# Optimization experiments

Hardware: AMD Instinct MI355X
Metric: run time of the kernel (lower is better)

The kernel has to match this reference:

```python
import jax, jax.numpy as jnp
import numpy as np

B, C, H, W = 8, 128, 64, 64
CQK = C // 8


def setup_inputs() -> dict:
    key = jax.random.key(0)
    ks = jax.random.split(key, 7)
    scale = 1.0 / np.sqrt(C)
    return {
        "x": jax.random.normal(ks[0], (B, C, H, W), dtype=jnp.float32),
        "wq": jax.random.normal(ks[1], (CQK, C), dtype=jnp.float32) * scale,
        "bq": jax.random.normal(ks[2], (CQK,), dtype=jnp.float32) * 0.01,
        "wk": jax.random.normal(ks[3], (CQK, C), dtype=jnp.float32) * scale,
        "bk": jax.random.normal(ks[4], (CQK,), dtype=jnp.float32) * 0.01,
        "wv": jax.random.normal(ks[5], (C, C), dtype=jnp.float32) * scale,
        "bv": jax.random.normal(ks[6], (C,), dtype=jnp.float32) * 0.01,
    }


def reference(x, wq, bq, wk, bk, wv, bv):
    b, c, h, w = x.shape
    n = h * w
    xf = x.reshape(b, c, n)                                  # [B,C,N]
    # 1x1 convs == channel matmuls
    q = jnp.einsum('oc,bcn->bon', wq, xf) + bq[:, None]      # [B,C/8,N]
    k = jnp.einsum('oc,bcn->bon', wk, xf) + bk[:, None]      # [B,C/8,N]
    v = jnp.einsum('oc,bcn->bon', wv, xf) + bv[:, None]      # [B,C,N]
    # energy[b,i,j] = <q[:,i], k[:,j]>  (note: NO 1/sqrt(d) scale, per source)
    energy = jnp.einsum('bci,bcj->bij', q, k)                # [B,N,N]
    att = jax.nn.softmax(energy, axis=-1)                    # softmax over j
    # out[b,c,i] = sum_j v[b,c,j] * att[b,i,j]
    out = jnp.einsum('bcj,bij->bci', v, att).reshape(b, c, h, w)
    return out + x
```

## Files before the change

kernel.cpp:

```cpp
#include <hip/hip_runtime.h>
#include <math.h>

#define NB  8
#define NC  128
#define NN  4096
#define NCQ 16
#define BI  64
#define BJ  64
#define NT  (NN / BJ)
#define WROWS 160

typedef __attribute__((ext_vector_type(8))) short short8v;
typedef __attribute__((ext_vector_type(4))) short short4v;
typedef __attribute__((ext_vector_type(4))) float f32x4;

__device__ __forceinline__ short f2bf(float f) {
    unsigned u = __builtin_bit_cast(unsigned, f);
    u += 0x7fffu + ((u >> 16) & 1u);
    return (short)(u >> 16);
}
__device__ __forceinline__ float bf2f(short h) {
    return __builtin_bit_cast(float, ((unsigned)(unsigned short)h) << 16);
}

__global__ __launch_bounds__(256) void wconv(
    const float* __restrict__ wq, const float* __restrict__ bq,
    const float* __restrict__ wk, const float* __restrict__ bk,
    const float* __restrict__ wv, const float* __restrict__ bv,
    short* __restrict__ whg, short* __restrict__ wlg, float* __restrict__ biasg)
{
    const int idx = blockIdx.x * 256 + threadIdx.x;
    if (idx < WROWS * NC) {
        const int row = idx >> 7, k = idx & 127;
        const float v = (row < 16) ? wq[row * NC + k]
                       : (row < 32) ? wk[(row - 16) * NC + k]
                                    : wv[(row - 32) * NC + k];
        const short h = f2bf(v);
        whg[idx] = h;
        wlg[idx] = f2bf(v - bf2f(h));
    }
    if (idx < WROWS)
        biasg[idx] = (idx < 16) ? bq[idx] : (idx < 32) ? bk[idx - 16] : bv[idx - 32];
}

__global__ __launch_bounds__(256) void qkv_gemm(
    const float* __restrict__ x,
    const short* __restrict__ whg, const short* __restrict__ wlg,
    const float* __restrict__ biasg,
    short* __restrict__ Qo, short* __restrict__ Ko, short* __restrict__ Vo)
{
    __shared__ __align__(16) short xsT[2][64][136];

    const int b  = blockIdx.y;
    const int n0 = blockIdx.x * 64;
    const int t  = threadIdx.x;
    const int w  = t >> 6;
    const int l  = t & 63;
    const int lr = l & 15;
    const int g  = l >> 4;

    const float* xb = x + (size_t)b * NC * NN;

#pragma unroll
    for (int it = 0; it < 8; ++it) {
        const int idx4 = t + 256 * it;
        const int cr = idx4 >> 4;
        const int j4 = (idx4 & 15) * 4;
        const float4 v = *reinterpret_cast<const float4*>(xb + (size_t)cr * NN + n0 + j4);
        const float vf[4] = {v.x, v.y, v.z, v.w};
#pragma unroll
        for (int p = 0; p < 4; ++p) {
            const short h = f2bf(vf[p]);
            xsT[0][j4 + p][cr] = h;
            xsT[1][j4 + p][cr] = f2bf(vf[p] - bf2f(h));
        }
    }
    __syncthreads();

    const int lc = 16 * w + lr;
    f32x4 acc[10];
#pragma unroll
    for (int rt = 0; rt < 10; ++rt) acc[rt] = {0.f, 0.f, 0.f, 0.f};

#pragma unroll
    for (int ks = 0; ks < 4; ++ks) {
        const short8v xh = *reinterpret_cast<const short8v*>(&xsT[0][lc][32 * ks + 8 * g]);
        const short8v xl = *reinterpret_cast<const short8v*>(&xsT[1][lc][32 * ks + 8 * g]);
#pragma unroll
        for (int rt = 0; rt < 10; ++rt) {
            const int wo = (16 * rt + lr) * NC + 32 * ks + 8 * g;
            const short8v ah = *reinterpret_cast<const short8v*>(whg + wo);
            const short8v al = *reinterpret_cast<const short8v*>(wlg + wo);
            acc[rt] = __builtin_amdgcn_mfma_f32_16x16x32_bf16(ah, xh, acc[rt], 0, 0, 0);
            acc[rt] = __builtin_amdgcn_mfma_f32_16x16x32_bf16(ah, xl, acc[rt], 0, 0, 0);
            acc[rt] = __builtin_amdgcn_mfma_f32_16x16x32_bf16(al, xh, acc[rt], 0, 0, 0);
        }
    }

    const int col = n0 + lc;
#pragma unroll
    for (int rt = 0; rt < 10; ++rt) {
#pragma unroll
        for (int r = 0; r < 4; ++r) {
            const int ch = 16 * rt + 4 * g + r;
            const short o = f2bf(acc[rt][r] + biasg[ch]);
            if (rt == 0)
                Qo[((size_t)b * NCQ + ch) * NN + col] = o;
            else if (rt == 1)
                Ko[((size_t)b * NCQ + (ch - 16)) * NN + col] = o;
            else
                Vo[((size_t)b * NC + (ch - 32)) * NN + col] = o;
        }
    }
}

__global__ __launch_bounds__(256) void attn_mfma(
    const short* __restrict__ Q, const short* __restrict__ K,
    const short* __restrict__ V, const float* __restrict__ x,
    float* __restrict__ out)
{
    __shared__ __align__(16) short ksT[2][BJ * 24];
    __shared__ __align__(16) short vsT[3][NC * BJ];
    __shared__ __align__(16) short psT[4][2][16 * BJ];

    const int b  = blockIdx.y;
    const int i0 = blockIdx.x * BI;
    const int t  = threadIdx.x;
    const int w  = t >> 6;
    const int l  = t & 63;
    const int lr = l & 15;
    const int g  = l >> 4;
    const int swz = (lr & 7) << 3;

    const short* Qb = Q + (size_t)b * NCQ * NN;
    const short* Kb = K + (size_t)b * NCQ * NN;
    const short* Vb = V + (size_t)b * NC * NN;

    const int ig = i0 + 16 * w + lr;

    const short8v kzero = {0, 0, 0, 0, 0, 0, 0, 0};
    const f32x4   fzero = {0.f, 0.f, 0.f, 0.f};

    const int kc  = t >> 4;
    const int kj4 = (t & 15) * 4;
    const int vc0 = t >> 3;
    const int vj8 = (t & 7) * 8;

    short4v kreg;
    short8v vreg0, vreg1, vreg2, vreg3;

#define LOAD_TILE(J0)                                                            \
    {                                                                            \
        kreg  = *reinterpret_cast<const short4v*>(Kb + (size_t)kc * NN + (J0) + kj4); \
        vreg0 = *reinterpret_cast<const short8v*>(Vb + (size_t)(vc0      ) * NN + (J0) + vj8); \
        vreg1 = *reinterpret_cast<const short8v*>(Vb + (size_t)(vc0 + 32 ) * NN + (J0) + vj8); \
        vreg2 = *reinterpret_cast<const short8v*>(Vb + (size_t)(vc0 + 64 ) * NN + (J0) + vj8); \
        vreg3 = *reinterpret_cast<const short8v*>(Vb + (size_t)(vc0 + 96 ) * NN + (J0) + vj8); \
    }
#define WRITE_TILE(KB_, VB_)                                                     \
    {                                                                            \
        _Pragma("unroll")                                                        \
        for (int p = 0; p < 4; ++p) ksT[KB_][(kj4 + p) * 24 + kc] = kreg[p];     \
        const int sw0 = vj8 ^ ((vc0 & 7) << 3);                                  \
        *reinterpret_cast<short8v*>(&vsT[VB_][(vc0      ) * BJ + sw0]) = vreg0;  \
        *reinterpret_cast<short8v*>(&vsT[VB_][(vc0 + 32 ) * BJ + sw0]) = vreg1;  \
        *reinterpret_cast<short8v*>(&vsT[VB_][(vc0 + 64 ) * BJ + sw0]) = vreg2;  \
        *reinterpret_cast<short8v*>(&vsT[VB_][(vc0 + 96 ) * BJ + sw0]) = vreg3;  \
    }
#define PV_STEP(PB_, VB_)                                                        \
    {                                                                            \
        __builtin_amdgcn_s_setprio(1);                                           \
        _Pragma("unroll")                                                        \
        for (int ks = 0; ks < 2; ++ks) {                                         \
            const int jb = (32 * ks + 8 * g) ^ swz;                              \
            const short8v pf = *reinterpret_cast<const short8v*>(                \
                    &psT[w][PB_][lr * BJ + jb]);                                 \
            _Pragma("unroll")                                                    \
            for (int cb = 0; cb < 8; ++cb) {                                     \
                const short8v vf = *reinterpret_cast<const short8v*>(            \
                        &vsT[VB_][(16 * cb + lr) * BJ + jb]);                    \
                acc[cb] = __builtin_amdgcn_mfma_f32_16x16x32_bf16(vf, pf, acc[cb], 0, 0, 0); \
            }                                                                    \
        }                                                                        \
        __builtin_amdgcn_s_setprio(0);                                           \
    }

    short8v qf = kzero;
    if (g < 2) {
        const short* qp = Qb + (size_t)(8 * g) * NN + ig;
#pragma unroll
        for (int e = 0; e < 8; ++e) qf[e] = qp[(size_t)e * NN];
    }

    float l_run = 0.f;
    f32x4 acc[8];
#pragma unroll
    for (int cb = 0; cb < 8; ++cb) acc[cb] = fzero;

    LOAD_TILE(0)
    WRITE_TILE(0, 0)
    __syncthreads();

    int vwr = 1;
    int vpv = 0;

    for (int jt = 0; jt < NT; ++jt) {
        const int kcur = jt & 1;
        if (jt < NT - 1) LOAD_TILE((jt + 1) * BJ)

        f32x4 e0, e1, e2, e3;
#define QK_TILE(ET, TT)                                                          \
        {                                                                        \
            short8v kf = kzero;                                                  \
            if (g < 2)                                                           \
                kf = *reinterpret_cast<const short8v*>(                          \
                        &ksT[kcur][(16 * (TT) + lr) * 24 + 8 * g]);              \
            ET = __builtin_amdgcn_mfma_f32_16x16x32_bf16(kf, qf, fzero, 0, 0, 0);\
        }
        QK_TILE(e0, 0) QK_TILE(e1, 1) QK_TILE(e2, 2) QK_TILE(e3, 3)
#undef QK_TILE

        float sum = 0.f;
#pragma unroll
        for (int r = 0; r < 4; ++r) { e0[r] = __expf(e0[r]); sum += e0[r]; }
#pragma unroll
        for (int r = 0; r < 4; ++r) { e1[r] = __expf(e1[r]); sum += e1[r]; }
#pragma unroll
        for (int r = 0; r < 4; ++r) { e2[r] = __expf(e2[r]); sum += e2[r]; }
#pragma unroll
        for (int r = 0; r < 4; ++r) { e3[r] = __expf(e3[r]); sum += e3[r]; }
        sum += __shfl_xor(sum, 16);
        sum += __shfl_xor(sum, 32);
        l_run += sum;

#define P_STORE(ET, TT)                                                           \
        {                                                                         \
            const int jb = 16 * (TT) + 4 * g;                                     \
            unsigned p01 = (unsigned short)f2bf(ET[0]) |                          \
                           ((unsigned)(unsigned short)f2bf(ET[1]) << 16);         \
            unsigned p23 = (unsigned short)f2bf(ET[2]) |                          \
                           ((unsigned)(unsigned short)f2bf(ET[3]) << 16);         \
            *reinterpret_cast<unsigned*>(&psT[w][kcur][lr * BJ + ( jb      ^ swz)]) = p01; \
            *reinterpret_cast<unsigned*>(&psT[w][kcur][lr * BJ + ((jb + 2) ^ swz)]) = p23; \
        }
        P_STORE(e0, 0) P_STORE(e1, 1) P_STORE(e2, 2) P_STORE(e3, 3)
#undef P_STORE

        if (jt > 0) {
            PV_STEP(kcur ^ 1, vpv)
            vpv = (vpv == 2) ? 0 : vpv + 1;
        }

        if (jt < NT - 1) {
            WRITE_TILE(kcur ^ 1, vwr)
            vwr = (vwr == 2) ? 0 : vwr + 1;
        }
        __syncthreads();
    }

    PV_STEP((NT - 1) & 1, vpv)

#undef LOAD_TILE
#undef WRITE_TILE
#undef PV_STEP

    const float inv = 1.f / l_run;
#pragma unroll
    for (int cb = 0; cb < 8; ++cb) {
#pragma unroll
        for (int r = 0; r < 4; ++r) {
            const int c = 16 * cb + 4 * g + r;
            const size_t o = ((size_t)b * NC + c) * NN + ig;
            out[o] = acc[cb][r] * inv + x[o];
        }
    }
}

extern "C" void kernel_launch(void* const* d_in, const int* in_sizes, int n_in,
                              void* d_out, int out_size, void* d_ws, size_t ws_size,
                              hipStream_t stream) {
    const float* x  = (const float*)d_in[0];
    const float* wq = (const float*)d_in[1];
    const float* bq = (const float*)d_in[2];
    const float* wk = (const float*)d_in[3];
    const float* bk = (const float*)d_in[4];
    const float* wv = (const float*)d_in[5];
    const float* bv = (const float*)d_in[6];
    float* out = (float*)d_out;

    short* ws = (short*)d_ws;
    short* Qo  = ws;
    short* Ko  = ws + (size_t)NB * NCQ * NN;
    short* Vo  = ws + 2 * (size_t)NB * NCQ * NN;
    short* whg = ws + 10 * (size_t)NB * NCQ * NN;
    short* wlg = whg + WROWS * NC;
    float* biasg = (float*)(wlg + WROWS * NC);

    wconv<<<dim3(80), 256, 0, stream>>>(wq, bq, wk, bk, wv, bv, whg, wlg, biasg);
    qkv_gemm<<<dim3(NN / 64, NB), 256, 0, stream>>>(x, whg, wlg, biasg, Qo, Ko, Vo);
    attn_mfma<<<dim3(NN / BI, NB), 256, 0, stream>>>(Qo, Ko, Vo, x, out);
}
```

Baseline: 193.3 us.

## Split attention work across waves by key tile and channel, read K/V directly from global

K is now written transposed ([N,16]) by the QKV GEMM, so each wave can load its K fragment straight from global memory. In the attention kernel each wave now computes energies for its own 16-column slice of the key tile against all 64 query rows. It shares P through LDS and does the PV product for a 32-channel slice, with V fragments loaded straight from global instead of staged in LDS. This removes the K/V LDS staging and the large vsT buffers and should raise occupancy. In exchange it adds uncoalesced V/K global loads per wave and a cross-wave row-sum reduction through LDS at the end.

```diff
diff --git a/kernel.cpp b/kernel.cpp
--- a/kernel.cpp
+++ b/kernel.cpp
@@ -47,7 +47,7 @@
     const float* __restrict__ x,
     const short* __restrict__ whg, const short* __restrict__ wlg,
     const float* __restrict__ biasg,
-    short* __restrict__ Qo, short* __restrict__ Ko, short* __restrict__ Vo)
+    short* __restrict__ Qo, short* __restrict__ KoT, short* __restrict__ Vo)
 {
     __shared__ __align__(16) short xsT[2][64][136];
 
@@ -107,7 +107,7 @@
             if (rt == 0)
                 Qo[((size_t)b * NCQ + ch) * NN + col] = o;
             else if (rt == 1)
-                Ko[((size_t)b * NCQ + (ch - 16)) * NN + col] = o;
+                KoT[((size_t)b * NN + col) * NCQ + (ch - 16)] = o;
             else
                 Vo[((size_t)b * NC + (ch - 32)) * NN + col] = o;
         }
@@ -115,13 +115,12 @@
 }
 
 __global__ __launch_bounds__(256) void attn_mfma(
-    const short* __restrict__ Q, const short* __restrict__ K,
+    const short* __restrict__ Q, const short* __restrict__ KT,
     const short* __restrict__ V, const float* __restrict__ x,
     float* __restrict__ out)
 {
-    __shared__ __align__(16) short ksT[2][BJ * 24];
-    __shared__ __align__(16) short vsT[3][NC * BJ];
-    __shared__ __align__(16) short psT[4][2][16 * BJ];
+    __shared__ __align__(16) short psT[2][64][72];
+    __shared__ float lsumX[4][4][16];
 
     const int b  = blockIdx.y;
     const int i0 = blockIdx.x * BI;
@@ -130,148 +129,153 @@
     const int l  = t & 63;
     const int lr = l & 15;
     const int g  = l >> 4;
-    const int swz = (lr & 7) << 3;
-
-    const short* Qb = Q + (size_t)b * NCQ * NN;
-    const short* Kb = K + (size_t)b * NCQ * NN;
-    const short* Vb = V + (size_t)b * NC * NN;
-
-    const int ig = i0 + 16 * w + lr;
+
+    const short* Qb  = Q  + (size_t)b * NCQ * NN;
+    const short* KTb = KT + (size_t)b * NN * NCQ;
+    const short* Vb  = V  + (size_t)b * NC * NN;
 
     const short8v kzero = {0, 0, 0, 0, 0, 0, 0, 0};
     const f32x4   fzero = {0.f, 0.f, 0.f, 0.f};
 
-    const int kc  = t >> 4;
-    const int kj4 = (t & 15) * 4;
-    const int vc0 = t >> 3;
-    const int vj8 = (t & 7) * 8;
-
-    short4v kreg;
-    short8v vreg0, vreg1, vreg2, vreg3;
-
-#define LOAD_TILE(J0)                                                            \
-    {                                                                            \
-        kreg  = *reinterpret_cast<const short4v*>(Kb + (size_t)kc * NN + (J0) + kj4); \
-        vreg0 = *reinterpret_cast<const short8v*>(Vb + (size_t)(vc0      ) * NN + (J0) + vj8); \
-        vreg1 = *reinterpret_cast<const short8v*>(Vb + (size_t)(vc0 + 32 ) * NN + (J0) + vj8); \
-        vreg2 = *reinterpret_cast<const short8v*>(Vb + (size_t)(vc0 + 64 ) * NN + (J0) + vj8); \
-        vreg3 = *reinterpret_cast<const short8v*>(Vb + (size_t)(vc0 + 96 ) * NN + (J0) + vj8); \
-    }
-#define WRITE_TILE(KB_, VB_)                                                     \
-    {                                                                            \
-        _Pragma("unroll")                                                        \
-        for (int p = 0; p < 4; ++p) ksT[KB_][(kj4 + p) * 24 + kc] = kreg[p];     \
-        const int sw0 = vj8 ^ ((vc0 & 7) << 3);                                  \
-        *reinterpret_cast<short8v*>(&vsT[VB_][(vc0      ) * BJ + sw0]) = vreg0;  \
-        *reinterpret_cast<short8v*>(&vsT[VB_][(vc0 + 32 ) * BJ + sw0]) = vreg1;  \
-        *reinterpret_cast<short8v*>(&vsT[VB_][(vc0 + 64 ) * BJ + sw0]) = vreg2;  \
-        *reinterpret_cast<short8v*>(&vsT[VB_][(vc0 + 96 ) * BJ + sw0]) = vreg3;  \
-    }
-#define PV_STEP(PB_, VB_)                                                        \
-    {                                                                            \
-        __builtin_amdgcn_s_setprio(1);                                           \
-        _Pragma("unroll")                                                        \
-        for (int ks = 0; ks < 2; ++ks) {                                         \
-            const int jb = (32 * ks + 8 * g) ^ swz;                              \
-            const short8v pf = *reinterpret_cast<const short8v*>(                \
-                    &psT[w][PB_][lr * BJ + jb]);                                 \
-            _Pragma("unroll")                                                    \
-            for (int cb = 0; cb < 8; ++cb) {                                     \
-                const short8v vf = *reinterpret_cast<const short8v*>(            \
-                        &vsT[VB_][(16 * cb + lr) * BJ + jb]);                    \
-                acc[cb] = __builtin_amdgcn_mfma_f32_16x16x32_bf16(vf, pf, acc[cb], 0, 0, 0); \
-            }                                                                    \
-        }                                                                        \
-        __builtin_amdgcn_s_setprio(0);                                           \
-    }
-
-    short8v qf = kzero;
+    short8v qf[4] = {kzero, kzero, kzero, kzero};
     if (g < 2) {
-        const short* qp = Qb + (size_t)(8 * g) * NN + ig;
-#pragma unroll
-        for (int e = 0; e < 8; ++e) qf[e] = qp[(size_t)e * NN];
-    }
-
-    float l_run = 0.f;
-    f32x4 acc[8];
-#pragma unroll
-    for (int cb = 0; cb < 8; ++cb) acc[cb] = fzero;
-
-    LOAD_TILE(0)
-    WRITE_TILE(0, 0)
-    __syncthreads();
-
-    int vwr = 1;
-    int vpv = 0;
+#pragma unroll
+        for (int it = 0; it < 4; ++it) {
+            const short* qp = Qb + (size_t)(8 * g) * NN + i0 + 16 * it + lr;
+#pragma unroll
+            for (int e = 0; e < 8; ++e) qf[it][e] = qp[(size_t)e * NN];
+        }
+    }
+
+    short8v kfA = kzero;
+    if (g < 2)
+        kfA = *reinterpret_cast<const short8v*>(KTb + (size_t)(16 * w + lr) * NCQ + 8 * g);
+
+    f32x4 acc[2][4];
+#pragma unroll
+    for (int ct = 0; ct < 2; ++ct)
+#pragma unroll
+        for (int it = 0; it < 4; ++it) acc[ct][it] = fzero;
+    float lsum[4] = {0.f, 0.f, 0.f, 0.f};
 
     for (int jt = 0; jt < NT; ++jt) {
-        const int kcur = jt & 1;
-        if (jt < NT - 1) LOAD_TILE((jt + 1) * BJ)
-
-        f32x4 e0, e1, e2, e3;
-#define QK_TILE(ET, TT)                                                          \
-        {                                                                        \
-            short8v kf = kzero;                                                  \
-            if (g < 2)                                                           \
-                kf = *reinterpret_cast<const short8v*>(                          \
-                        &ksT[kcur][(16 * (TT) + lr) * 24 + 8 * g]);              \
-            ET = __builtin_amdgcn_mfma_f32_16x16x32_bf16(kf, qf, fzero, 0, 0, 0);\
-        }
-        QK_TILE(e0, 0) QK_TILE(e1, 1) QK_TILE(e2, 2) QK_TILE(e3, 3)
-#undef QK_TILE
-
-        float sum = 0.f;
-#pragma unroll
-        for (int r = 0; r < 4; ++r) { e0[r] = __expf(e0[r]); sum += e0[r]; }
-#pragma unroll
-        for (int r = 0; r < 4; ++r) { e1[r] = __expf(e1[r]); sum += e1[r]; }
-#pragma unroll
-        for (int r = 0; r < 4; ++r) { e2[r] = __expf(e2[r]); sum += e2[r]; }
-#pragma unroll
-        for (int r = 0; r < 4; ++r) { e3[r] = __expf(e3[r]); sum += e3[r]; }
-        sum += __shfl_xor(sum, 16);
-        sum += __shfl_xor(sum, 32);
-        l_run += sum;
-
-#define P_STORE(ET, TT)                                                           \
+        const int cur = jt & 1;
+
+        short8v kfB = kzero;
+        if (jt + 1 < NT && g < 2)
+            kfB = *reinterpret_cast<const short8v*>(
+                    KTb + (size_t)((jt + 1) * BJ + 16 * w + lr) * NCQ + 8 * g);
+
+        short8v vf00, vf01, vf10, vf11;
+        if (jt > 0) {
+            const short* vp = Vb + (size_t)(32 * w + lr) * NN + (jt - 1) * BJ + 8 * g;
+            vf00 = *reinterpret_cast<const short8v*>(vp);
+            vf01 = *reinterpret_cast<const short8v*>(vp + 32);
+            vf10 = *reinterpret_cast<const short8v*>(vp + 16 * NN);
+            vf11 = *reinterpret_cast<const short8v*>(vp + 16 * NN + 32);
+        }
+
+        f32x4 e0 = __builtin_amdgcn_mfma_f32_16x16x32_bf16(kfA, qf[0], fzero, 0, 0, 0);
+        f32x4 e1 = __builtin_amdgcn_mfma_f32_16x16x32_bf16(kfA, qf[1], fzero, 0, 0, 0);
+        f32x4 e2 = __builtin_amdgcn_mfma_f32_16x16x32_bf16(kfA, qf[2], fzero, 0, 0, 0);
+        f32x4 e3 = __builtin_amdgcn_mfma_f32_16x16x32_bf16(kfA, qf[3], fzero, 0, 0, 0);
+
+#pragma unroll
+        for (int r = 0; r < 4; ++r) e0[r] = __expf(e0[r]);
+#pragma unroll
+        for (int r = 0; r < 4; ++r) e1[r] = __expf(e1[r]);
+#pragma unroll
+        for (int r = 0; r < 4; ++r) e2[r] = __expf(e2[r]);
+#pragma unroll
+        for (int r = 0; r < 4; ++r) e3[r] = __expf(e3[r]);
+        lsum[0] += (e0[0] + e0[1]) + (e0[2] + e0[3]);
+        lsum[1] += (e1[0] + e1[1]) + (e1[2] + e1[3]);
+        lsum[2] += (e2[0] + e2[1]) + (e2[2] + e2[3]);
+        lsum[3] += (e3[0] + e3[1]) + (e3[2] + e3[3]);
+
+        if (jt > 0) {
+            const int prev = cur ^ 1;
+            __builtin_amdgcn_s_setprio(1);
+#pragma unroll
+            for (int ks = 0; ks < 2; ++ks) {
+#pragma unroll
+                for (int it = 0; it < 4; ++it) {
+                    const short8v pf = *reinterpret_cast<const short8v*>(
+                            &psT[prev][16 * it + lr][32 * ks + 8 * g]);
+                    acc[0][it] = __builtin_amdgcn_mfma_f32_16x16x32_bf16(
+                            ks ? vf01 : vf00, pf, acc[0][it], 0, 0, 0);
+                    acc[1][it] = __builtin_amdgcn_mfma_f32_16x16x32_bf16(
+                            ks ? vf11 : vf10, pf, acc[1][it], 0, 0, 0);
+                }
+            }
+            __builtin_amdgcn_s_setprio(0);
+        }
+
+#define P_STORE(ET, IT)                                                           \
         {                                                                         \
-            const int jb = 16 * (TT) + 4 * g;                                     \
             unsigned p01 = (unsigned short)f2bf(ET[0]) |                          \
                            ((unsigned)(unsigned short)f2bf(ET[1]) << 16);         \
             unsigned p23 = (unsigned short)f2bf(ET[2]) |                          \
                            ((unsigned)(unsigned short)f2bf(ET[3]) << 16);         \
-            *reinterpret_cast<unsigned*>(&psT[w][kcur][lr * BJ + ( jb      ^ swz)]) = p01; \
-            *reinterpret_cast<unsigned*>(&psT[w][kcur][lr * BJ + ((jb + 2) ^ swz)]) = p23; \
+            *reinterpret_cast<unsigned*>(&psT[cur][16 * (IT) + lr][16 * w + 4 * g])     = p01; \
+            *reinterpret_cast<unsigned*>(&psT[cur][16 * (IT) + lr][16 * w + 4 * g + 2]) = p23; \
         }
         P_STORE(e0, 0) P_STORE(e1, 1) P_STORE(e2, 2) P_STORE(e3, 3)
 #undef P_STORE
 
-        if (jt > 0) {
-            PV_STEP(kcur ^ 1, vpv)
-            vpv = (vpv == 2) ? 0 : vpv + 1;
-        }
-
-        if (jt < NT - 1) {
-            WRITE_TILE(kcur ^ 1, vwr)
-            vwr = (vwr == 2) ? 0 : vwr + 1;
-        }
         __syncthreads();
-    }
-
-    PV_STEP((NT - 1) & 1, vpv)
-
-#undef LOAD_TILE
-#undef WRITE_TILE
-#undef PV_STEP
-
-    const float inv = 1.f / l_run;
-#pragma unroll
-    for (int cb = 0; cb < 8; ++cb) {
-#pragma unroll
-        for (int r = 0; r < 4; ++r) {
-            const int c = 16 * cb + 4 * g + r;
-            const size_t o = ((size_t)b * NC + c) * NN + ig;
-            out[o] = acc[cb][r] * inv + x[o];
+        kfA = kfB;
+    }
+
+    {
+        const int prev = (NT - 1) & 1;
+        const short* vp = Vb + (size_t)(32 * w + lr) * NN + (NT - 1) * BJ + 8 * g;
+        const short8v vf00 = *reinterpret_cast<const short8v*>(vp);
+        const short8v vf01 = *reinterpret_cast<const short8v*>(vp + 32);
+        const short8v vf10 = *reinterpret_cast<const short8v*>(vp + 16 * NN);
+        const short8v vf11 = *reinterpret_cast<const short8v*>(vp + 16 * NN + 32);
+#pragma unroll
+        for (int ks = 0; ks < 2; ++ks) {
+#pragma unroll
+            for (int it = 0; it < 4; ++it) {
+                const short8v pf = *reinterpret_cast<const short8v*>(
+                        &psT[prev][16 * it + lr][32 * ks + 8 * g]);
+                acc[0][it] = __builtin_amdgcn_mfma_f32_16x16x32_bf16(
+                        ks ? vf01 : vf00, pf, acc[0][it], 0, 0, 0);
+                acc[1][it] = __builtin_amdgcn_mfma_f32_16x16x32_bf16(
+                        ks ? vf11 : vf10, pf, acc[1][it], 0, 0, 0);
+            }
+        }
+    }
+
+#pragma unroll
+    for (int it = 0; it < 4; ++it) {
+        lsum[it] += __shfl_xor(lsum[it], 16);
+        lsum[it] += __shfl_xor(lsum[it], 32);
+    }
+    if (l < 16) {
+#pragma unroll
+        for (int it = 0; it < 4; ++it) lsumX[w][it][l] = lsum[it];
+    }
+    __syncthreads();
+    float inv[4];
+#pragma unroll
+    for (int it = 0; it < 4; ++it) {
+        const float lr_tot = (lsumX[0][it][lr] + lsumX[1][it][lr]) +
+                             (lsumX[2][it][lr] + lsumX[3][it][lr]);
+        inv[it] = 1.f / lr_tot;
+    }
+
+#pragma unroll
+    for (int ct = 0; ct < 2; ++ct) {
+#pragma unroll
+        for (int it = 0; it < 4; ++it) {
+#pragma unroll
+            for (int r = 0; r < 4; ++r) {
+                const int c = 32 * w + 16 * ct + 4 * g + r;
+                const size_t o = ((size_t)b * NC + c) * NN + i0 + 16 * it + lr;
+                out[o] = acc[ct][it][r] * inv[it] + x[o];
+            }
         }
     }
 }
@@ -290,13 +294,13 @@
 
     short* ws = (short*)d_ws;
     short* Qo  = ws;
-    short* Ko  = ws + (size_t)NB * NCQ * NN;
+    short* KoT = ws + (size_t)NB * NCQ * NN;
     short* Vo  = ws + 2 * (size_t)NB * NCQ * NN;
     short* whg = ws + 10 * (size_t)NB * NCQ * NN;
     short* wlg = whg + WROWS * NC;
     float* biasg = (float*)(wlg + WROWS * NC);
 
     wconv<<<dim3(80), 256, 0, stream>>>(wq, bq, wk, bk, wv, bv, whg, wlg, biasg);
-    qkv_gemm<<<dim3(NN / 64, NB), 256, 0, stream>>>(x, whg, wlg, biasg, Qo, Ko, Vo);
-    attn_mfma<<<dim3(NN / BI, NB), 256, 0, stream>>>(Qo, Ko, Vo, x, out);
-}
+    qkv_gemm<<<dim3(NN / 64, NB), 256, 0, stream>>>(x, whg, wlg, biasg, Qo, KoT, Vo);
+    attn_mfma<<<dim3(NN / BI, NB), 256, 0, stream>>>(Qo, KoT, Vo, x, out);
+}
```

Result: faster. 174.6 us (-9.7%).
